# Kernel optimization log

Hardware: AMD Instinct MI355X
Metric: run time of the kernel (lower is better)

The kernel has to match this reference:

```python
import jax, jax.numpy as jnp
import numpy as np

IN_FEATURES = 2048
OUT_FEATURES = 2048
TOP_K = 1024


def setup_inputs() -> dict:
    key = jax.random.key(0)
    kx, kw, kb = jax.random.split(key, 3)
    bound = 1.0 / np.sqrt(IN_FEATURES)
    x = jax.random.normal(kx, (8, 2048, IN_FEATURES), dtype=jnp.float32)
    weight = jax.random.uniform(kw, (OUT_FEATURES, IN_FEATURES), dtype=jnp.float32,
                                minval=-bound, maxval=bound)
    bias = jax.random.uniform(kb, (OUT_FEATURES,), dtype=jnp.float32,
                              minval=-bound, maxval=bound)
    return {"x": x, "weight": weight, "bias": bias}


def _topk_mask(weight: jnp.ndarray, k: int) -> jnp.ndarray:
    # Per output row, keep the k largest-magnitude weights (binary mask).
    _, idx = jax.lax.top_k(jnp.abs(weight), k)            # [out, k]
    rows = jnp.arange(weight.shape[0])[:, None]            # [out, 1]
    mask = jnp.zeros_like(weight).at[rows, idx].set(1.0)   # scatter ones
    return mask


def reference(x, weight, bias):
    # y = x @ (mask * W)^T + b, mask = top-k by |W| per output feature
    mask = _topk_mask(weight, TOP_K)
    masked_weight = weight * mask                          # [out, in]
    return jnp.einsum('bsi,oi->bso', x, masked_weight) + bias
```

## Files before the change

### kernel.cpp

```cpp
#include <hip/hip_runtime.h>

typedef __attribute__((ext_vector_type(8))) short s16x8;
typedef __attribute__((ext_vector_type(4))) float f32x4;
typedef __attribute__((ext_vector_type(8))) unsigned short u16x8;

#define GLB(p) ((const __attribute__((address_space(1))) void*)(p))
#define LDS(p) ((__attribute__((address_space(3))) void*)(p))

__device__ __forceinline__ unsigned short f2bf(float f) {
  unsigned u = __float_as_uint(f);
  u += 0x7fffu + ((u >> 16) & 1u);
  return (unsigned short)(u >> 16);
}

__global__ __launch_bounds__(256) void prep_kernel(
    const float* __restrict__ W, unsigned short* __restrict__ Wb,
    const float* __restrict__ X, unsigned short* __restrict__ Xb) {
  __shared__ int hist[4096];
  __shared__ int scanres[2];
  __shared__ int wsum[4];
  const int tid  = threadIdx.x;

  if (blockIdx.x >= 2048) {
    const size_t i = ((size_t)(blockIdx.x - 2048) * 256 + tid) * 8;
    const float4* xp = (const float4*)(X + i);
    const float4 a = xp[0], b = xp[1];
    u16x8 o;
    o[0] = f2bf(a.x); o[1] = f2bf(a.y); o[2] = f2bf(a.z); o[3] = f2bf(a.w);
    o[4] = f2bf(b.x); o[5] = f2bf(b.y); o[6] = f2bf(b.z); o[7] = f2bf(b.w);
    *(u16x8*)(Xb + i) = o;
    return;
  }

  const int lane = tid & 63;
  const int wv   = tid >> 6;
  const int row  = blockIdx.x;
  const float* wr = W + (size_t)row * 2048;

  const float4 v0 = *(const float4*)(wr + tid * 8);
  const float4 v1 = *(const float4*)(wr + tid * 8 + 4);
  float val[8] = {v0.x, v0.y, v0.z, v0.w, v1.x, v1.y, v1.z, v1.w};
  unsigned key[8];
#pragma unroll
  for (int e = 0; e < 8; ++e) key[e] = __float_as_uint(val[e]) & 0x7fffffffu;

  unsigned prefix = 0;
  int rem = 1024;

  for (int i = tid; i < 4096; i += 256) hist[i] = 0;
  __syncthreads();
#pragma unroll
  for (int e = 0; e < 8; ++e) atomicAdd(&hist[key[e] >> 20], 1);
  __syncthreads();
  if (wv == 0) {
    const int base = 4096 - (lane + 1) * 64;
    int s = 0;
    for (int b = 0; b < 64; ++b) s += hist[base + b];
    int cum = s;
#pragma unroll
    for (int off = 1; off < 64; off <<= 1) {
      int o = __shfl_up(cum, off, 64);
      if (lane >= off) cum += o;
    }
    const int cumex = cum - s;
    if (cumex < rem && rem <= cum) {
      int running = cumex;
      for (int b = 63; b >= 0; --b) {
        int h = hist[base + b];
        if (running + h >= rem) { scanres[0] = base + b; scanres[1] = rem - running; break; }
        running += h;
      }
    }
  }
  __syncthreads();
  prefix = ((unsigned)scanres[0]) << 20;
  rem = scanres[1];
  __syncthreads();

  for (int i = tid; i < 1024; i += 256) hist[i] = 0;
  __syncthreads();
#pragma unroll
  for (int e = 0; e < 8; ++e)
    if ((key[e] >> 20) == (prefix >> 20)) atomicAdd(&hist[(key[e] >> 10) & 1023], 1);
  __syncthreads();
  if (wv == 0) {
    const int base = 1024 - (lane + 1) * 16;
    int s = 0;
    for (int b = 0; b < 16; ++b) s += hist[base + b];
    int cum = s;
#pragma unroll
    for (int off = 1; off < 64; off <<= 1) {
      int o = __shfl_up(cum, off, 64);
      if (lane >= off) cum += o;
    }
    const int cumex = cum - s;
    if (cumex < rem && rem <= cum) {
      int running = cumex;
      for (int b = 15; b >= 0; --b) {
        int h = hist[base + b];
        if (running + h >= rem) { scanres[0] = base + b; scanres[1] = rem - running; break; }
        running += h;
      }
    }
  }
  __syncthreads();
  prefix |= ((unsigned)scanres[0]) << 10;
  rem = scanres[1];
  __syncthreads();

  for (int i = tid; i < 1024; i += 256) hist[i] = 0;
  __syncthreads();
#pragma unroll
  for (int e = 0; e < 8; ++e)
    if ((key[e] >> 10) == (prefix >> 10)) atomicAdd(&hist[key[e] & 1023], 1);
  __syncthreads();
  if (wv == 0) {
    const int base = 1024 - (lane + 1) * 16;
    int s = 0;
    for (int b = 0; b < 16; ++b) s += hist[base + b];
    int cum = s;
#pragma unroll
    for (int off = 1; off < 64; off <<= 1) {
      int o = __shfl_up(cum, off, 64);
      if (lane >= off) cum += o;
    }
    const int cumex = cum - s;
    if (cumex < rem && rem <= cum) {
      int running = cumex;
      for (int b = 15; b >= 0; --b) {
        int h = hist[base + b];
        if (running + h >= rem) { scanres[0] = base + b; scanres[1] = rem - running; break; }
        running += h;
      }
    }
  }
  __syncthreads();
  const unsigned T = prefix | (unsigned)scanres[0];
  rem = scanres[1];

  int eqcnt = 0;
#pragma unroll
  for (int e = 0; e < 8; ++e) eqcnt += (key[e] == T) ? 1 : 0;
  int c = eqcnt;
#pragma unroll
  for (int off = 1; off < 64; off <<= 1) {
    int o = __shfl_up(c, off, 64);
    if (lane >= off) c += o;
  }
  if (lane == 63) wsum[wv] = c;
  __syncthreads();
  int wavebase = 0;
  for (int j = 0; j < wv; ++j) wavebase += wsum[j];
  const int myex = wavebase + c - eqcnt;

  u16x8 o;
  int r = 0;
#pragma unroll
  for (int e = 0; e < 8; ++e) {
    const bool iseq = (key[e] == T);
    const bool keep = (key[e] > T) || (iseq && (myex + r) < rem);
    r += iseq ? 1 : 0;
    o[e] = keep ? f2bf(val[e]) : (unsigned short)0;
  }
  *(u16x8*)(Wb + (size_t)row * 2048 + tid * 8) = o;
}

__global__ __launch_bounds__(256) void gemm_bt_kernel(
    const unsigned short* __restrict__ A,
    const unsigned short* __restrict__ B,
    const float* __restrict__ bias,
    float* __restrict__ C) {
  constexpr int K = 2048;
  constexpr int N = 2048;
  __shared__ __align__(16) unsigned short lA[128 * 64];
  __shared__ __align__(16) unsigned short lB[128 * 64];

  const int tid  = threadIdx.x;
  const int lane = tid & 63;
  const int wv   = tid >> 6;

  const int lin = blockIdx.y * 16 + blockIdx.x;
  const int st = lin >> 4, wi = lin & 15;
  const int tile_n = (st & 3) * 4 + (wi & 3);
  const int tile_m = (st >> 2) * 4 + (wi >> 2);

  const int wm = (wv >> 1) * 64;
  const int wn = (wv & 1) * 64;

  f32x4 acc[4][4] = {};

  const int srow = lane >> 3;
  const int sxor = ((lane & 7) ^ srow) * 8;
  const unsigned short* gA0 = A + (size_t)(tile_m * 128 + wv * 8 + srow) * K + sxor;
  const unsigned short* gB0 = B + (size_t)(tile_n * 128 + wv * 8 + srow) * K + sxor;
  const size_t rstep = (size_t)32 * K;
  unsigned short* lAq[4];
  unsigned short* lBq[4];
#pragma unroll
  for (int q = 0; q < 4; ++q) {
    lAq[q] = &lA[(q * 32 + wv * 8) * 64];
    lBq[q] = &lB[(q * 32 + wv * 8) * 64];
  }

  const int fr = lane & 15;
  const int qw = lane >> 4;
  const int x0 = ((qw ^ (fr & 7))) * 8;
  const int x1 = x0 ^ 32;
  const unsigned short* la_f = &lA[(wm + fr) * 64];
  const unsigned short* lb_f = &lB[(wn + fr) * 64];

  for (int k0 = 0; k0 < K; k0 += 64) {
#pragma unroll
    for (int q = 0; q < 4; ++q) {
      __builtin_amdgcn_global_load_lds(GLB(gA0 + q * rstep + k0), LDS(lAq[q]), 16, 0, 0);
      __builtin_amdgcn_global_load_lds(GLB(gB0 + q * rstep + k0), LDS(lBq[q]), 16, 0, 0);
    }
    __syncthreads();

#pragma unroll
    for (int kk = 0; kk < 2; ++kk) {
      const int xo = kk ? x1 : x0;
      s16x8 af[4], bf[4];
#pragma unroll
      for (int i = 0; i < 4; ++i)
        af[i] = *(const s16x8*)&la_f[i * 16 * 64 + xo];
#pragma unroll
      for (int j = 0; j < 4; ++j)
        bf[j] = *(const s16x8*)&lb_f[j * 16 * 64 + xo];
#pragma unroll
      for (int i = 0; i < 4; ++i)
#pragma unroll
        for (int j = 0; j < 4; ++j)
          acc[i][j] = __builtin_amdgcn_mfma_f32_16x16x32_bf16(af[i], bf[j], acc[i][j], 0, 0, 0);
    }
    __syncthreads();
  }

  float bv[4];
#pragma unroll
  for (int j = 0; j < 4; ++j)
    bv[j] = bias[tile_n * 128 + wn + j * 16 + (lane & 15)];

  float* Cp = C + (size_t)(tile_m * 128 + wm + (lane >> 4) * 4) * N
                + tile_n * 128 + wn + (lane & 15);
#pragma unroll
  for (int i = 0; i < 4; ++i)
#pragma unroll
    for (int j = 0; j < 4; ++j)
#pragma unroll
      for (int r = 0; r < 4; ++r)
        Cp[(size_t)(i * 16 + r) * N + j * 16] = acc[i][j][r] + bv[j];
}

extern "C" void kernel_launch(void* const* d_in, const int* in_sizes, int n_in,
                              void* d_out, int out_size, void* d_ws, size_t ws_size,
                              hipStream_t stream) {
  const float* x    = (const float*)d_in[0];
  const float* w    = (const float*)d_in[1];
  const float* bias = (const float*)d_in[2];
  float* out = (float*)d_out;

  constexpr int M = 8 * 2048;
  constexpr int N = 2048;
  constexpr int K = 2048;

  unsigned short* xb = (unsigned short*)d_ws;
  unsigned short* wb = xb + (size_t)M * K;

  const int conv_blocks = ((size_t)M * K) / (256 * 8);
  prep_kernel<<<2048 + conv_blocks, 256, 0, stream>>>(w, wb, x, xb);
  gemm_bt_kernel<<<dim3(N / 128, M / 128), 256, 0, stream>>>(xb, wb, bias, out);
}
```

Measured before the change: 376.6 us.

## Rewrite GEMM as 256x256 tiles with 8 waves and double-buffered LDS pipeline

The bf16 GEMM moves from 128x128 tiles with 4 waves and single-buffered LDS to 256x256 tiles with 8 waves and 128KB of double-buffered LDS. Global-to-LDS loads for later k-steps are issued between four MFMA phases, using explicit waitcnt, barriers and setprio so memory traffic overlaps compute. This aims to raise arithmetic intensity and hide load latency. In exchange it adds larger register pressure, many barriers per iteration, and fragile manual wait counts.

```diff
diff --git a/kernel.cpp b/kernel.cpp
--- a/kernel.cpp
+++ b/kernel.cpp
@@ -6,6 +6,10 @@
 
 #define GLB(p) ((const __attribute__((address_space(1))) void*)(p))
 #define LDS(p) ((__attribute__((address_space(3))) void*)(p))
+
+#define BAR() __builtin_amdgcn_s_barrier()
+#define LGKM(n) asm volatile("s_waitcnt lgkmcnt(" #n ")" ::: "memory")
+#define VMC(n) asm volatile("s_waitcnt vmcnt(" #n ")" ::: "memory")
 
 __device__ __forceinline__ unsigned short f2bf(float f) {
   unsigned u = __float_as_uint(f);
@@ -165,91 +169,176 @@
   *(u16x8*)(Wb + (size_t)row * 2048 + tid * 8) = o;
 }
 
-__global__ __launch_bounds__(256) void gemm_bt_kernel(
+__global__ __launch_bounds__(512, 2) void gemm_bt_kernel(
     const unsigned short* __restrict__ A,
     const unsigned short* __restrict__ B,
     const float* __restrict__ bias,
     float* __restrict__ C) {
   constexpr int K = 2048;
   constexpr int N = 2048;
-  __shared__ __align__(16) unsigned short lA[128 * 64];
-  __shared__ __align__(16) unsigned short lB[128 * 64];
-
-  const int tid  = threadIdx.x;
-  const int lane = tid & 63;
-  const int wv   = tid >> 6;
-
-  const int lin = blockIdx.y * 16 + blockIdx.x;
-  const int st = lin >> 4, wi = lin & 15;
-  const int tile_n = (st & 3) * 4 + (wi & 3);
-  const int tile_m = (st >> 2) * 4 + (wi >> 2);
-
-  const int wm = (wv >> 1) * 64;
-  const int wn = (wv & 1) * 64;
-
-  f32x4 acc[4][4] = {};
-
-  const int srow = lane >> 3;
-  const int sxor = ((lane & 7) ^ srow) * 8;
-  const unsigned short* gA0 = A + (size_t)(tile_m * 128 + wv * 8 + srow) * K + sxor;
-  const unsigned short* gB0 = B + (size_t)(tile_n * 128 + wv * 8 + srow) * K + sxor;
-  const size_t rstep = (size_t)32 * K;
-  unsigned short* lAq[4];
-  unsigned short* lBq[4];
-#pragma unroll
-  for (int q = 0; q < 4; ++q) {
-    lAq[q] = &lA[(q * 32 + wv * 8) * 64];
-    lBq[q] = &lB[(q * 32 + wv * 8) * 64];
-  }
-
-  const int fr = lane & 15;
-  const int qw = lane >> 4;
-  const int x0 = ((qw ^ (fr & 7))) * 8;
-  const int x1 = x0 ^ 32;
-  const unsigned short* la_f = &lA[(wm + fr) * 64];
-  const unsigned short* lb_f = &lB[(wn + fr) * 64];
-
-  for (int k0 = 0; k0 < K; k0 += 64) {
-#pragma unroll
-    for (int q = 0; q < 4; ++q) {
-      __builtin_amdgcn_global_load_lds(GLB(gA0 + q * rstep + k0), LDS(lAq[q]), 16, 0, 0);
-      __builtin_amdgcn_global_load_lds(GLB(gB0 + q * rstep + k0), LDS(lBq[q]), 16, 0, 0);
-    }
-    __syncthreads();
-
-#pragma unroll
-    for (int kk = 0; kk < 2; ++kk) {
-      const int xo = kk ? x1 : x0;
-      s16x8 af[4], bf[4];
+  constexpr int T = K / 64;
+  constexpr size_t HK = (size_t)128 * K;
+
+  __shared__ __align__(16) char lds_[131072];
+
+  const int tid = threadIdx.x;
+  const int l   = tid & 63;
+  const int wv  = tid >> 6;
+  const int wm  = wv & 1;
+  const int wn  = wv >> 1;
+
+  const int lin = blockIdx.x;
+  const int o   = (lin & 7) * 64 + (lin >> 3);
+  const int tm  = o >> 3;
+  const int tn  = o & 7;
+
+  int rS[2], cS[2];
+#pragma unroll
+  for (int e = 0; e < 2; ++e) {
+    const int d   = (e * 512 + tid) * 16;
+    const int off = d ^ (((d >> 9) & 1) << 5);
+    rS[e] = ((off >> 11) << 4) | ((off >> 6) & 15);
+    cS[e] = (((off >> 10) & 1) << 5) | (((off >> 4) & 3) << 3);
+  }
+  const unsigned short* const pA0 = A + (size_t)(tm * 256 + rS[0]) * K + cS[0];
+  const unsigned short* const pA1 = A + (size_t)(tm * 256 + rS[1]) * K + cS[1];
+  const unsigned short* const pB0 = B + (size_t)(tn * 256 + rS[0]) * K + cS[0];
+  const unsigned short* const pB1 = B + (size_t)(tn * 256 + rS[1]) * K + cS[1];
+
+  auto stage = [&](const unsigned short* g0, const unsigned short* g1, char* d) {
+    __builtin_amdgcn_global_load_lds(GLB(g0), LDS(d + wv * 1024), 16, 0, 0);
+    __builtin_amdgcn_global_load_lds(GLB(g1), LDS(d + 8192 + wv * 1024), 16, 0, 0);
+  };
+
+  const int laneoff = (((l & 15) << 6) | ((l >> 4) << 4)) ^ ((l & 8) << 2);
+  const char* const aRd = (const char*)lds_ + wm * 2048 + laneoff;
+  const char* const bRd = (const char*)lds_ + 65536 + wn * 2048 + laneoff;
+
+  f32x4 acc[8][4] = {};
+
+  stage(pA0,            pA1,            lds_);
+  stage(pB0 + HK,       pB1 + HK,       lds_ + 65536 + 16384);
+  stage(pA0 + HK,       pA1 + HK,       lds_ + 16384);
+  stage(pB0,            pB1,            lds_ + 65536);
+  stage(pA0 + 64,       pA1 + 64,       lds_ + 32768);
+  stage(pB0 + HK + 64,  pB1 + HK + 64,  lds_ + 65536 + 32768 + 16384);
+  stage(pA0 + HK + 64,  pA1 + HK + 64,  lds_ + 32768 + 16384);
+  VMC(6);
+  BAR();
+
+  for (int t = 0; t < T; ++t) {
+    const int bb = t & 1;
+    const char* aT = aRd + bb * 32768;
+    const char* bT = bRd + bb * 32768;
+    char* sA  = lds_ + bb * 32768;
+    char* sB  = lds_ + 65536 + bb * 32768;
+    char* sBn = lds_ + 65536 + (bb ^ 1) * 32768;
+
+    s16x8 af[4][2], f0[2][2], f1[2][2];
+
+#pragma unroll
+    for (int i = 0; i < 4; ++i) {
+      af[i][0] = *(const s16x8*)(aT + i * 4096);
+      af[i][1] = *(const s16x8*)(aT + i * 4096 + 1024);
+    }
+#pragma unroll
+    for (int j = 0; j < 2; ++j) {
+      f0[j][0] = *(const s16x8*)(bT + j * 8192);
+      f0[j][1] = *(const s16x8*)(bT + j * 8192 + 1024);
+    }
+    if (t + 1 < T)
+      stage(pB0 + (size_t)(t + 1) * 64, pB1 + (size_t)(t + 1) * 64, sBn);
+    LGKM(8);
+    BAR();
+    LGKM(0);
+    __builtin_amdgcn_s_setprio(1);
+#pragma unroll
+    for (int kk = 0; kk < 2; ++kk)
 #pragma unroll
       for (int i = 0; i < 4; ++i)
-        af[i] = *(const s16x8*)&la_f[i * 16 * 64 + xo];
-#pragma unroll
-      for (int j = 0; j < 4; ++j)
-        bf[j] = *(const s16x8*)&lb_f[j * 16 * 64 + xo];
+#pragma unroll
+        for (int j = 0; j < 2; ++j)
+          acc[i][j] = __builtin_amdgcn_mfma_f32_16x16x32_bf16(af[i][kk], f0[j][kk], acc[i][j], 0, 0, 0);
+    __builtin_amdgcn_s_setprio(0);
+    BAR();
+
+#pragma unroll
+    for (int j = 0; j < 2; ++j) {
+      f1[j][0] = *(const s16x8*)(bT + 16384 + j * 8192);
+      f1[j][1] = *(const s16x8*)(bT + 16384 + j * 8192 + 1024);
+    }
+    if (t + 2 < T)
+      stage(pA0 + (size_t)(t + 2) * 64, pA1 + (size_t)(t + 2) * 64, sA);
+    BAR();
+    LGKM(0);
+    __builtin_amdgcn_s_setprio(1);
+#pragma unroll
+    for (int kk = 0; kk < 2; ++kk)
 #pragma unroll
       for (int i = 0; i < 4; ++i)
 #pragma unroll
-        for (int j = 0; j < 4; ++j)
-          acc[i][j] = __builtin_amdgcn_mfma_f32_16x16x32_bf16(af[i], bf[j], acc[i][j], 0, 0, 0);
-    }
-    __syncthreads();
+        for (int j = 0; j < 2; ++j)
+          acc[i][j + 2] = __builtin_amdgcn_mfma_f32_16x16x32_bf16(af[i][kk], f1[j][kk], acc[i][j + 2], 0, 0, 0);
+    __builtin_amdgcn_s_setprio(0);
+    BAR();
+
+#pragma unroll
+    for (int i = 0; i < 4; ++i) {
+      af[i][0] = *(const s16x8*)(aT + 16384 + i * 4096);
+      af[i][1] = *(const s16x8*)(aT + 16384 + i * 4096 + 1024);
+    }
+    if (t + 2 < T)
+      stage(pB0 + HK + (size_t)(t + 2) * 64, pB1 + HK + (size_t)(t + 2) * 64, sB + 16384);
+    BAR();
+    LGKM(0);
+    __builtin_amdgcn_s_setprio(1);
+#pragma unroll
+    for (int kk = 0; kk < 2; ++kk)
+#pragma unroll
+      for (int i = 0; i < 4; ++i)
+#pragma unroll
+        for (int j = 0; j < 2; ++j)
+          acc[i + 4][j + 2] = __builtin_amdgcn_mfma_f32_16x16x32_bf16(af[i][kk], f1[j][kk], acc[i + 4][j + 2], 0, 0, 0);
+    __builtin_amdgcn_s_setprio(0);
+    BAR();
+
+#pragma unroll
+    for (int j = 0; j < 2; ++j) {
+      f0[j][0] = *(const s16x8*)(bT + j * 8192);
+      f0[j][1] = *(const s16x8*)(bT + j * 8192 + 1024);
+    }
+    if (t + 2 < T)
+      stage(pA0 + HK + (size_t)(t + 2) * 64, pA1 + HK + (size_t)(t + 2) * 64, sA + 16384);
+    BAR();
+    LGKM(0);
+    __builtin_amdgcn_s_setprio(1);
+#pragma unroll
+    for (int kk = 0; kk < 2; ++kk)
+#pragma unroll
+      for (int i = 0; i < 4; ++i)
+#pragma unroll
+        for (int j = 0; j < 2; ++j)
+          acc[i + 4][j] = __builtin_amdgcn_mfma_f32_16x16x32_bf16(af[i][kk], f0[j][kk], acc[i + 4][j], 0, 0, 0);
+    __builtin_amdgcn_s_setprio(0);
+    if (t + 2 < T) { VMC(6); } else { VMC(0); }
+    BAR();
   }
 
   float bv[4];
 #pragma unroll
   for (int j = 0; j < 4; ++j)
-    bv[j] = bias[tile_n * 128 + wn + j * 16 + (lane & 15)];
-
-  float* Cp = C + (size_t)(tile_m * 128 + wm + (lane >> 4) * 4) * N
-                + tile_n * 128 + wn + (lane & 15);
-#pragma unroll
-  for (int i = 0; i < 4; ++i)
+    bv[j] = bias[tn * 256 + (4 * j + wn) * 16 + (l & 15)];
+
+  const int crow0 = tm * 256 + wm * 16 + (l >> 4) * 4;
+  const int ccol0 = tn * 256 + wn * 16 + (l & 15);
+  float* Cp = C + (size_t)crow0 * N + ccol0;
+#pragma unroll
+  for (int i = 0; i < 8; ++i)
 #pragma unroll
     for (int j = 0; j < 4; ++j)
 #pragma unroll
       for (int r = 0; r < 4; ++r)
-        Cp[(size_t)(i * 16 + r) * N + j * 16] = acc[i][j][r] + bv[j];
+        Cp[(size_t)(i * 32 + r) * N + j * 64] = acc[i][j][r] + bv[j];
 }
 
 extern "C" void kernel_launch(void* const* d_in, const int* in_sizes, int n_in,
@@ -269,5 +358,5 @@
 
   const int conv_blocks = ((size_t)M * K) / (256 * 8);
   prep_kernel<<<2048 + conv_blocks, 256, 0, stream>>>(w, wb, x, xb);
-  gemm_bt_kernel<<<dim3(N / 128, M / 128), 256, 0, stream>>>(xb, wb, bias, out);
+  gemm_bt_kernel<<<(M / 256) * (N / 256), 512, 0, stream>>>(xb, wb, bias, out);
 }
```

Result: faster. 356.7 us (-5.3%).
